# Kernel tuning notes

Hardware: AMD Instinct MI355X
Metric: run time of the kernel (lower is better)

Reference implementation:

```python
import jax, jax.numpy as jnp
import numpy as np
from jax import lax

T, B = 32, 32
GRID = (16, 16)
N_ACT = 5
CNN_DIM = 512
MAP_DIM = CNN_DIM + N_ACT  # 517
FLAT = MAP_DIM * GRID[0] * GRID[1]  # 132352


def _conv(x, w, b, stride):
    y = lax.conv_general_dilated(x, w, (stride, stride), 'VALID',
                                 dimension_numbers=('NCHW', 'OIHW', 'NCHW'))
    return jax.nn.relu(y + b[None, :, None, None])


def setup_inputs() -> dict:
    key = jax.random.key(0)
    ks = jax.random.split(key, 16)
    inp = {
        'image': jax.random.uniform(ks[0], (T * B, 3, 64, 64), jnp.float32),
        'last_action': jax.random.randint(ks[1], (T * B,), 0, N_ACT),
        'position': jax.random.randint(ks[2], (T * B, 2), 0, GRID[0]),
        'done': jnp.zeros((T, B), jnp.float32),
        'state0': jnp.zeros((B, MAP_DIM, GRID[0], GRID[1]), jnp.float32),
        'c1_w': jax.random.normal(ks[3], (32, 3, 8, 8), jnp.float32) * 0.05,
        'c1_b': jnp.zeros((32,), jnp.float32),
        'c2_w': jax.random.normal(ks[4], (64, 32, 4, 4), jnp.float32) * 0.05,
        'c2_b': jnp.zeros((64,), jnp.float32),
        'c3_w': jax.random.normal(ks[5], (64, 64, 3, 3), jnp.float32) * 0.05,
        'c3_b': jnp.zeros((64,), jnp.float32),
        'fc_w': jax.random.normal(ks[6], (CNN_DIM, 1024), jnp.float32) * 0.03,
        'fc_b': jnp.zeros((CNN_DIM,), jnp.float32),
        'pol_w1': jax.random.normal(ks[7], (64, FLAT), jnp.float32) * 0.005,
        'pol_b1': jnp.zeros((64,), jnp.float32),
        'pol_w2': jax.random.normal(ks[8], (N_ACT, 64), jnp.float32) * 0.01,
        'pol_b2': jnp.zeros((N_ACT,), jnp.float32),
        'val_w1': jax.random.normal(ks[9], (64, FLAT), jnp.float32) * 0.005,
        'val_b1': jnp.zeros((64,), jnp.float32),
        'val_w2': jax.random.normal(ks[10], (1, 64), jnp.float32) * 0.01,
        'val_b2': jnp.zeros((1,), jnp.float32),
    }
    return inp


def reference(image, last_action, position, done, state0,
              c1_w, c1_b, c2_w, c2_b, c3_w, c3_b, fc_w, fc_b,
              pol_w1, pol_b1, pol_w2, pol_b2, val_w1, val_b1, val_w2, val_b2):
    # NatureCNN feature extractor (image already normalized to [0,1])
    x = _conv(image, c1_w, c1_b, 4)   # (TB,32,15,15)
    x = _conv(x, c2_w, c2_b, 2)       # (TB,64,6,6)
    x = _conv(x, c3_w, c3_b, 1)       # (TB,64,4,4)
    feat = jax.nn.relu(x.reshape(x.shape[0], -1) @ fc_w.T + fc_b)  # (TB,512)
    onehot = jax.nn.one_hot(last_action, N_ACT, dtype=feat.dtype)
    h = jnp.concatenate([feat, onehot], axis=1)       # (TB,517)

    h_seq = h.reshape(T, B, MAP_DIM)
    idx_seq = position.reshape(T, B, 2)
    benv = jnp.arange(B)

    def step(state, inp):
        ht, dt, it = inp
        masked = (1.0 - dt)[:, None, None, None] * state      # reset done envs
        new_state = masked.at[benv, :, it[:, 0], it[:, 1]].set(ht)  # scatter write
        return new_state, new_state.reshape(B, -1)

    final_state, outs = lax.scan(step, state0, (h_seq, done, idx_seq))
    hidden = outs.reshape(T * B, FLAT)

    logits = jnp.tanh(hidden @ pol_w1.T + pol_b1) @ pol_w2.T + pol_b2  # (TB,5)
    v = jnp.tanh(hidden @ val_w1.T + val_b1) @ val_w2.T + val_b2       # (TB,1)
    return logits, v, final_state
```

## Files before the change

### kernel.cpp

```cpp
#include <hip/hip_runtime.h>

#define T_ 32
#define B_ 32
#define MAPD 517
#define P_ 256
#define FLATD (MAPD*P_)
#define TBN (T_*B_)

typedef unsigned short u16;
typedef unsigned int u32;
typedef __attribute__((ext_vector_type(4))) short short4v;
typedef __attribute__((ext_vector_type(8))) short short8v;
typedef __attribute__((ext_vector_type(4))) float f32x4;
typedef __attribute__((ext_vector_type(2))) float f32x2;
typedef __attribute__((ext_vector_type(4))) u32 u32x4;

__device__ __forceinline__ float bfv(u16 u){ u32 x = ((u32)u)<<16; return __uint_as_float(x); }
__device__ __forceinline__ u16 fbf(float f){
  u32 x = __float_as_uint(f);
  return (u16)((x + 0x7fffu + ((x>>16)&1u))>>16);
}
template<bool F32> __device__ __forceinline__ float ld(const void* p, size_t i){
  if constexpr (F32) return ((const float*)p)[i];
  else               return bfv(((const u16*)p)[i]);
}

__global__ void k_probe(const void* img, int* flag){
  if (threadIdx.x == 0 && blockIdx.x == 0){
    const u16* u = (const u16*)img;
    int cnt = 0;
    for (int i = 0; i < 256; ++i) if (u[i] <= 0x4380u) ++cnt;
    *flag = (cnt < 240) ? 1 : 0;
  }
}

__global__ __launch_bounds__(256) void k_prep(const void* c1w, const void* c2w, const void* c3w,
                                              const void* fcw, const void* st0,
                                              u16* W1F, u16* W2F, u16* W3F, u16* FWF, u16* ST0T,
                                              const int* flag){
  __shared__ __align__(16) char smem_[32768];
  bool f32 = (*flag != 0);
  int bid = blockIdx.x, tid = threadIdx.x;
  if (bid < 24){
    int idx = bid*256 + tid;
    int j = idx & 7, l = (idx>>3) & 63, t = idx>>9;
    int nt = t/6, s = t - nt*6;
    int oc = nt*16 + (l&15);
    int kk = 8*(4*s + (l>>4)) + j;
    float v = f32 ? ((const float*)c1w)[oc*192+kk] : bfv(((const u16*)c1w)[oc*192+kk]);
    W1F[idx] = fbf(v);
  } else if (bid < 152){
    int idx = (bid-24)*256 + tid;
    int j = idx & 7, l = (idx>>3) & 63, s = (idx>>9) & 15, nt = idx>>13;
    int oc = nt*16 + (l&15);
    int cin = (l>>4)*8 + j;
    int src = oc*512 + cin*16 + (s>>2)*4 + (s&3);
    float v = f32 ? ((const float*)c2w)[src] : bfv(((const u16*)c2w)[src]);
    W2F[idx] = fbf(v);
  } else if (bid < 296){
    int idx = (bid-152)*256 + tid;
    int j = idx & 7, l = (idx>>3) & 63, t = idx>>9;
    int nt = t/18, s = t - nt*18;
    int oc = nt*16 + (l&15);
    int c = (s&1)*32 + (l>>4)*8 + j;
    int src = oc*576 + c*9 + (s>>1);
    float v = f32 ? ((const float*)c3w)[src] : bfv(((const u16*)c3w)[src]);
    W3F[idx] = fbf(v);
  } else if (bid < 424){
    int b = bid - 296;
    for (int it = 0; it < 16; ++it){
      int idx = (b*16 + it)*256 + tid;
      int j = idx & 7, l = (idx>>3) & 63, frag = idx >> 9;
      int nt = frag >> 5, kt = frag & 31;
      int kc = kt*32 + ((l>>4)<<3) + j;
      int kr = (kc & 63)*16 + (kc >> 6);
      int o  = nt*16 + (l & 15);
      float v = f32 ? ((const float*)fcw)[(size_t)o*1024 + kr]
                    : bfv(((const u16*)fcw)[(size_t)o*1024 + kr]);
      FWF[idx] = fbf(v);
    }
  } else {
    u16* tile = (u16*)smem_;
    int b0 = bid - 424;
    int c0 = (b0 >> 2)*8, p0 = (b0 & 3)*64;
    for (int it = 0; it < 64; ++it){
      int idx = it*256 + tid;
      int pl = idx & 63, b = (idx>>6)&31, ci = idx>>11;
      int c = c0 + ci;
      float v = 0.f;
      if (c < MAPD)
        v = f32 ? ((const float*)st0)[((size_t)b*MAPD+c)*256 + p0+pl]
                : bfv(((const u16*)st0)[((size_t)b*MAPD+c)*256 + p0+pl]);
      tile[ci*2048 + pl*32 + b] = fbf(v);
    }
    __syncthreads();
    for (int it = 0; it < 64; ++it){
      int idx = it*256 + tid;
      int b = idx & 31, ci = (idx>>5)&7, pl = idx>>8;
      int c = c0 + ci;
      if (c < MAPD)
        ST0T[((size_t)(p0+pl)*MAPD + c)*32 + b] = tile[ci*2048 + pl*32 + b];
    }
  }
}

__global__ void k_meta(const int* pos, const void* done, const int* lact,
                       int* prev, float* coef, float* H, int* lastw, float* lastc, const int* flag){
  bool f32 = (*flag != 0);
  int bid = blockIdx.x;
  if (bid < 4){
    int i = bid*256 + threadIdx.x;
    int t = i >> 5, b = i & 31;
    int p = pos[i*2]*16 + pos[i*2+1];
    int pv = -1;
    for (int s = t-1; s >= 0; --s){
      int n = s*32 + b;
      if (pos[n*2]*16 + pos[n*2+1] == p){ pv = s; break; }
    }
    float cf = 1.f;
    for (int s = (pv<0?0:pv+1); s <= t-1; ++s)
      cf *= (1.f - (f32 ? ((const float*)done)[s*32+b] : bfv(((const u16*)done)[s*32+b])));
    prev[i] = pv; coef[i] = cf;
    int la = lact[i];
    #pragma unroll
    for (int a = 0; a < 5; ++a) H[(size_t)i*MAPD + 512 + a] = (la == a) ? 1.f : 0.f;
  } else {
    int i = (bid-4)*256 + threadIdx.x;
    int b = i >> 8, p = i & 255;
    int lw = -1;
    for (int s = T_-1; s >= 0; --s){
      int n = s*32 + b;
      if (pos[n*2]*16 + pos[n*2+1] == p){ lw = s; break; }
    }
    float cf = 1.f;
    for (int s = (lw<0?0:lw+1); s < T_; ++s)
      cf *= (1.f - (f32 ? ((const float*)done)[s*32+b] : bfv(((const u16*)done)[s*32+b])));
    lastw[i] = lw; lastc[i] = cf;
  }
}

__global__ __launch_bounds__(256) void k_conv123(const void* img,
                                                 const u16* __restrict__ W1F, const void* b1,
                                                 const u16* __restrict__ W2F, const void* b2,
                                                 const u16* __restrict__ W3F, const void* b3,
                                                 u16* __restrict__ out, const int* flag){
  __shared__ __align__(16) u16 smem[19488];
  u16* sImg = smem;
  u16* sA   = smem + 12288;
  u16* sBv  = smem;
  bool f32 = (*flag != 0);
  int n = blockIdx.x, tid = threadIdx.x;
  if (f32){
    const float4* ip = (const float4*)((const float*)img + (size_t)n*12288);
    for (int i = tid; i < 3072; i += 256){
      float4 v = ip[i];
      ushort4 u; u.x = fbf(v.x); u.y = fbf(v.y); u.z = fbf(v.z); u.w = fbf(v.w);
      int L = i*4;
      int addr = (L & ~63) | (((L & 63) + (((L >> 6) & 3) << 4)) & 63);
      *(ushort4*)(sImg + addr) = u;
    }
  } else {
    const ushort4* ip = (const ushort4*)((const u16*)img + (size_t)n*12288);
    for (int i = tid; i < 3072; i += 256){
      ushort4 u = ip[i];
      int L = i*4;
      int addr = (L & ~63) | (((L & 63) + (((L >> 6) & 3) << 4)) & 63);
      *(ushort4*)(sImg + addr) = u;
    }
  }
  int wv = tid >> 6, lane = tid & 63;
  int mi = lane & 15, q = lane >> 4;

  short8v bfr1[2][6];
  #pragma unroll
  for (int nt = 0; nt < 2; ++nt)
    #pragma unroll
    for (int s = 0; s < 6; ++s)
      bfr1[nt][s] = ((const short8v*)W1F)[(nt*6+s)*64 + lane];
  float b1v[2];
  #pragma unroll
  for (int nt = 0; nt < 2; ++nt)
    b1v[nt] = f32 ? ((const float*)b1)[nt*16+mi] : bfv(((const u16*)b1)[nt*16+mi]);
  __syncthreads();

  {
    f32x4 acc[4][2];
    #pragma unroll
    for (int mt = 0; mt < 4; ++mt)
      #pragma unroll
      for (int nt = 0; nt < 2; ++nt)
        acc[mt][nt] = (f32x4){0.f,0.f,0.f,0.f};
    int base[4];
    #pragma unroll
    for (int mt = 0; mt < 4; ++mt){
      int m = (wv*4+mt)*16 + mi;
      int mc = m < 225 ? m : 224;
      int oy = mc/15, ox = mc - oy*15;
      base[mt] = oy*256 + ox*4;
    }
    for (int s = 0; s < 6; ++s){
      int cky = 4*s + q;
      int off = (cky >> 3)*4096 + (cky & 7)*64;
      #pragma unroll
      for (int mt = 0; mt < 4; ++mt){
        int Lb = base[mt] + off;
        const u16* rp = sImg + (Lb & ~63);
        int x0 = Lb & 63;
        int rot = ((Lb >> 6) & 3) << 4;
        short4v lo = *(const short4v*)(rp + ((x0 + rot) & 63));
        short4v hi = *(const short4v*)(rp + ((x0 + 4 + rot) & 63));
        short8v a = __builtin_shufflevector(lo, hi, 0,1,2,3,4,5,6,7);
        acc[mt][0] = __builtin_amdgcn_mfma_f32_16x16x32_bf16(a, bfr1[0][s], acc[mt][0], 0,0,0);
        acc[mt][1] = __builtin_amdgcn_mfma_f32_16x16x32_bf16(a, bfr1[1][s], acc[mt][1], 0,0,0);
      }
    }
    __syncthreads();
    #pragma unroll
    for (int mt = 0; mt < 4; ++mt){
      int mrow0 = (wv*4+mt)*16 + q*4;
      #pragma unroll
      for (int nt = 0; nt < 2; ++nt){
        int oc = nt*16 + mi;
        #pragma unroll
        for (int r = 0; r < 4; ++r){
          int m = mrow0 + r;
          if (m < 225){
            int g = ((oc >> 3) ^ ((m >> 1) & 3)) << 3;
            sA[m*32 + g + (oc & 7)] = fbf(fmaxf(acc[mt][nt][r] + b1v[nt], 0.f));
          }
        }
      }
    }
  }
  __syncthreads();

  {
    short8v bfr2[16];
    #pragma unroll
    for (int s = 0; s < 16; ++s)
      bfr2[s] = ((const short8v*)W2F)[(wv*16+s)*64 + lane];
    int oc = wv*16 + mi;
    float bv = f32 ? ((const float*)b2)[oc] : bfv(((const u16*)b2)[oc]);
    f32x4 acc[3];
    #pragma unroll
    for (int mt = 0; mt < 3; ++mt) acc[mt] = (f32x4){0.f,0.f,0.f,0.f};
    int pixb[3];
    #pragma unroll
    for (int mt = 0; mt < 3; ++mt){
      int m = mt*16 + mi; if (m > 35) m = 35;
      int oy = m/6, ox = m - oy*6;
      pixb[mt] = oy*30 + ox*2;
    }
    #pragma unroll
    for (int s = 0; s < 16; ++s){
      int dp = (s>>2)*15 + (s&3);
      #pragma unroll
      for (int mt = 0; mt < 3; ++mt){
        int pix = pixb[mt] + dp;
        int g = (q ^ ((pix >> 1) & 3)) << 3;
        short8v a = *(const short8v*)(sA + pix*32 + g);
        acc[mt] = __builtin_amdgcn_mfma_f32_16x16x32_bf16(a, bfr2[s], acc[mt], 0,0,0);
      }
    }
    __syncthreads();
    #pragma unroll
    for (int mt = 0; mt < 3; ++mt)
      #pragma unroll
      for (int r = 0; r < 4; ++r){
        int m = mt*16 + q*4 + r;
        if (m < 36){
          int g = ((oc >> 3) ^ (m & 7)) << 3;
          sBv[m*64 + g + (oc & 7)] = fbf(fmaxf(acc[mt][r] + bv, 0.f));
        }
      }
  }
  __syncthreads();

  {
    int oy = mi >> 2, ox = mi & 3;
    int oc = wv*16 + mi;
    float bv = f32 ? ((const float*)b3)[oc] : bfv(((const u16*)b3)[oc]);
    short8v bfr3[18];
    #pragma unroll
    for (int s = 0; s < 18; ++s)
      bfr3[s] = ((const short8v*)W3F)[(wv*18+s)*64 + lane];
    f32x4 acc = (f32x4){0.f,0.f,0.f,0.f};
    #pragma unroll
    for (int s = 0; s < 18; ++s){
      int pair = s >> 1, ky = pair/3, kx = pair - ky*3;
      int pix = (oy+ky)*6 + ox+kx;
      int g = ((((s & 1) << 2) | q) ^ (pix & 7)) << 3;
      short8v a = *(const short8v*)(sBv + pix*64 + g);
      acc = __builtin_amdgcn_mfma_f32_16x16x32_bf16(a, bfr3[s], acc, 0,0,0);
    }
    u16* ob = out + (size_t)n*1024;
    #pragma unroll
    for (int r = 0; r < 4; ++r)
      ob[(q*4+r)*64 + oc] = fbf(fmaxf(acc[r] + bv, 0.f));
  }
}

__global__ __launch_bounds__(256) void k_fc(const u16* __restrict__ C, const u16* __restrict__ FWF,
                                            const void* fb, float* __restrict__ H, const int* flag){
  bool f32 = (*flag != 0);
  int wv = threadIdx.x >> 6, lane = threadIdx.x & 63;
  int mi = lane & 15, q = lane >> 4;
  int mt = blockIdx.x >> 3;
  int nt = (blockIdx.x & 7)*4 + wv;
  const u16* ap = C + (size_t)(mt*16 + mi)*1024 + q*8;
  const short8v* bp = (const short8v*)FWF + (size_t)nt*32*64 + lane;
  f32x4 acc0 = (f32x4){0.f,0.f,0.f,0.f};
  f32x4 acc1 = (f32x4){0.f,0.f,0.f,0.f};
  #pragma unroll
  for (int kt = 0; kt < 32; kt += 2){
    short8v a0 = *(const short8v*)(ap + kt*32);
    short8v b0 = bp[kt*64];
    short8v a1 = *(const short8v*)(ap + (kt+1)*32);
    short8v b1 = bp[(kt+1)*64];
    acc0 = __builtin_amdgcn_mfma_f32_16x16x32_bf16(a0, b0, acc0, 0,0,0);
    acc1 = __builtin_amdgcn_mfma_f32_16x16x32_bf16(a1, b1, acc1, 0,0,0);
  }
  int o = nt*16 + mi;
  float bv = f32 ? ((const float*)fb)[o] : bfv(((const u16*)fb)[o]);
  #pragma unroll
  for (int r = 0; r < 4; ++r){
    int m = mt*16 + q*4 + r;
    H[(size_t)m*MAPD + o] = fmaxf(acc0[r] + acc1[r] + bv, 0.f);
  }
}

template<bool F32> __device__ void wt_body(const void* pw1, const void* vw1, u16* wt, u32* tile){
  int c  = blockIdx.x >> 1;
  int ph = blockIdx.x & 1;
  for (int it = 0; it < 4; ++it){
    int idx = it*256 + threadIdx.x;
    int jp = idx >> 4, pg = idx & 15;
    int j0 = jp*2;
    const void* w = (j0 < 64) ? pw1 : vw1;
    int jj0 = (j0 < 64) ? j0 : j0-64;
    size_t base0 = (size_t)jj0*FLATD + c*P_ + ph*128 + pg*8;
    size_t base1 = base0 + FLATD;
    u16 a[8], b[8];
    if constexpr (F32){
      const float* f = (const float*)w;
      float4 a0 = *(const float4*)(f + base0), a1 = *(const float4*)(f + base0 + 4);
      float4 b0 = *(const float4*)(f + base1), b1 = *(const float4*)(f + base1 + 4);
      a[0]=fbf(a0.x); a[1]=fbf(a0.y); a[2]=fbf(a0.z); a[3]=fbf(a0.w);
      a[4]=fbf(a1.x); a[5]=fbf(a1.y); a[6]=fbf(a1.z); a[7]=fbf(a1.w);
      b[0]=fbf(b0.x); b[1]=fbf(b0.y); b[2]=fbf(b0.z); b[3]=fbf(b0.w);
      b[4]=fbf(b1.x); b[5]=fbf(b1.y); b[6]=fbf(b1.z); b[7]=fbf(b1.w);
    } else {
      short8v va = *(const short8v*)((const u16*)w + base0);
      short8v vb = *(const short8v*)((const u16*)w + base1);
      #pragma unroll
      for (int k = 0; k < 8; ++k){ a[k] = (u16)va[k]; b[k] = (u16)vb[k]; }
    }
    int slot = (jp >> 2) ^ pg;
    int sub  = jp & 3;
    #pragma unroll
    for (int k = 0; k < 8; ++k){
      int pp = pg*8 + k;
      tile[pp*64 + slot*4 + sub] = (u32)a[k] | ((u32)b[k] << 16);
    }
  }
  __syncthreads();
  for (int it = 0; it < 8; ++it){
    int idx = it*256 + threadIdx.x;
    int pp = idx >> 4, jb = idx & 15;
    int slot = jb ^ ((pp >> 3) & 15);
    u32x4 v = *(const u32x4*)(tile + pp*64 + slot*4);
    int p = ph*128 + pp;
    *(u32x4*)(wt + ((size_t)p*MAPD + c)*128 + jb*8) = v;
  }
}
__global__ __launch_bounds__(256) void k_wt(const void* pw1, const void* vw1, u16* wt, const int* flag){
  __shared__ u32 tile[128*64];
  if (*flag) wt_body<true>(pw1,vw1,wt,tile); else wt_body<false>(pw1,vw1,wt,tile);
}

template<int CLEN>
__device__ __forceinline__ void yloop(const u16* __restrict__ wp, const float* __restrict__ sSb,
                                      float (&acc)[8][2]){
  #pragma unroll 10
  for (int c = 0; c < CLEN; ++c){
    u32 w = *(const u32*)(wp + (size_t)c*128);
    float w0 = bfv((u16)(w & 0xffffu)), w1 = bfv((u16)(w >> 16));
    const float4* s4 = (const float4*)(sSb + c*32);
    float4 sa = s4[0], sb = s4[1];
    float sv[8] = {sa.x,sa.y,sa.z,sa.w,sb.x,sb.y,sb.z,sb.w};
    #pragma unroll
    for (int bb = 0; bb < 8; ++bb){
      acc[bb][0] += sv[bb]*w0;
      acc[bb][1] += sv[bb]*w1;
    }
  }
}
__global__ __launch_bounds__(256) void k_yinit(const u16* __restrict__ ST0T, const u16* __restrict__ wt,
                                               u16* __restrict__ PARTB){
  __shared__ float sS[130*32];
  int p = blockIdx.x >> 2, cq = blockIdx.x & 3;
  int c0 = cq*130;
  int clen = (cq == 3) ? 127 : 130;
  const ushort4* ssrc = (const ushort4*)(ST0T + ((size_t)p*MAPD + c0)*32);
  int n4 = clen*8;
  for (int i = threadIdx.x; i < n4; i += 256){
    ushort4 u = ssrc[i];
    float4 f; f.x = bfv(u.x); f.y = bfv(u.y); f.z = bfv(u.z); f.w = bfv(u.w);
    *(float4*)(sS + i*4) = f;
  }
  __syncthreads();
  int jg = threadIdx.x & 63, bg = threadIdx.x >> 6;
  int j0 = jg*2, b0 = bg*8;
  const u16* wp = wt + ((size_t)p*MAPD + c0)*128 + j0;
  float acc[8][2] = {};
  if (cq < 3) yloop<130>(wp, sS + b0, acc);
  else        yloop<127>(wp, sS + b0, acc);
  u32* op = (u32*)(PARTB + (size_t)blockIdx.x*4096);
  #pragma unroll
  for (int bb = 0; bb < 8; ++bb){
    u32 pk = (u32)fbf(acc[bb][0]) | ((u32)fbf(acc[bb][1]) << 16);
    op[((b0+bb)*128 + j0) >> 1] = pk;
  }
}

__global__ __launch_bounds__(256) void k_yred(const u16* __restrict__ PARTB, float* __restrict__ YI){
  int o = blockIdx.x*64 + (threadIdx.x & 63);
  int kq = threadIdx.x >> 6;
  float s = 0.f;
  const u16* pp = PARTB + (size_t)kq*256*4096 + o;
  #pragma unroll 8
  for (int k = 0; k < 256; ++k) s += bfv(pp[(size_t)k*4096]);
  __shared__ float red[256];
  red[threadIdx.x] = s;
  __syncthreads();
  if (threadIdx.x < 64)
    YI[o] = red[threadIdx.x] + red[threadIdx.x+64] + red[threadIdx.x+128] + red[threadIdx.x+192];
}

__global__ __launch_bounds__(128) void k_delta(const float* __restrict__ H, const u16* __restrict__ wt,
                                               const u16* __restrict__ st0t,
                                               const int* __restrict__ pos, const void* done,
                                               const int* __restrict__ prev, const float* __restrict__ coef,
                                               float* __restrict__ dlt8, const int* flag){
  __shared__ float diff[132];
  bool f32 = (*flag != 0);
  int n = blockIdx.x >> 2, cq = blockIdx.x & 3;
  int c0 = cq*130, clen = (cq == 3) ? 127 : 130;
  int b = n & 31;
  int p = pos[n*2]*16 + pos[n*2+1];
  float dn = f32 ? ((const float*)done)[n] : bfv(((const u16*)done)[n]);
  float m = 1.f - dn;
  int pv = prev[n];
  float cf = coef[n]*m;
  const float* hc = H + (size_t)n*MAPD + c0;
  for (int c = threadIdx.x; c < clen; c += 128){
    float old;
    if (pv >= 0) old = H[(size_t)(pv*32 + b)*MAPD + c0 + c];
    else         old = bfv(st0t[((size_t)p*MAPD + c0 + c)*32 + b]);
    diff[c] = hc[c] - cf*old;
  }
  __syncthreads();
  int half = threadIdx.x >> 6, jp = threadIdx.x & 63, j0 = jp*2;
  int hbase, hlen;
  if (cq == 3){ hbase = half*64; hlen = half ? 63 : 64; }
  else        { hbase = half*65; hlen = 65; }
  const u16* wp = wt + ((size_t)p*MAPD + c0 + hbase)*128 + j0;
  const float* dptr = diff + hbase;
  float a0 = 0.f, a1 = 0.f;
  int c = 0;
  for (; c + 4 <= hlen; c += 4){
    u32 w0 = *(const u32*)(wp + (size_t)(c+0)*128);
    u32 w1 = *(const u32*)(wp + (size_t)(c+1)*128);
    u32 w2 = *(const u32*)(wp + (size_t)(c+2)*128);
    u32 w3 = *(const u32*)(wp + (size_t)(c+3)*128);
    float d0 = dptr[c], d1 = dptr[c+1], d2 = dptr[c+2], d3 = dptr[c+3];
    a0 += d0*bfv((u16)(w0 & 0xffffu)) + d1*bfv((u16)(w1 & 0xffffu))
        + d2*bfv((u16)(w2 & 0xffffu)) + d3*bfv((u16)(w3 & 0xffffu));
    a1 += d0*bfv((u16)(w0 >> 16)) + d1*bfv((u16)(w1 >> 16))
        + d2*bfv((u16)(w2 >> 16)) + d3*bfv((u16)(w3 >> 16));
  }
  for (; c < hlen; ++c){
    u32 w = *(const u32*)(wp + (size_t)c*128);
    a0 += dptr[c]*bfv((u16)(w & 0xffffu));
    a1 += dptr[c]*bfv((u16)(w >> 16));
  }
  f32x2 st; st[0] = a0; st[1] = a1;
  *(f32x2*)(dlt8 + ((size_t)blockIdx.x*2 + half)*128 + j0) = st;
}

__global__ __launch_bounds__(128) void k_scan(const float* __restrict__ yi,
                                              const float* __restrict__ dlt8, const void* done,
                                              const void* pb1, const void* vb1,
                                              float* __restrict__ TH, const int* flag){
  bool f32 = (*flag != 0);
  int b = blockIdx.x, j = threadIdx.x;
  float y = yi[b*128 + j];
  float bias = (j < 64) ? (f32 ? ((const float*)pb1)[j]    : bfv(((const u16*)pb1)[j]))
                        : (f32 ? ((const float*)vb1)[j-64] : bfv(((const u16*)vb1)[j-64]));
  for (int t = 0; t < T_; ++t){
    int n = t*32 + b;
    float m = 1.f - (f32 ? ((const float*)done)[n] : bfv(((const u16*)done)[n]));
    const float* dp = dlt8 + (size_t)n*1024 + j;
    float d = dp[0] + dp[128] + dp[256] + dp[384]
            + dp[512] + dp[640] + dp[768] + dp[896];
    y = m*y + d;
    TH[(size_t)n*128 + j] = tanhf(y + bias);
  }
}

__global__ __launch_bounds__(256) void k_heads(const float* __restrict__ TH,
                                               const void* pw2, const void* pb2,
                                               const void* vw2, const void* vb2,
                                               void* out, const int* flag){
  bool f32 = (*flag != 0);
  int wv = threadIdx.x >> 6, lane = threadIdx.x & 63;
  int n = blockIdx.x*4 + wv;
  const float* th = TH + (size_t)n*128;
  float tq = th[lane];
  float tv = th[64 + lane];
  float acc[6];
  #pragma unroll
  for (int j = 0; j < 5; ++j)
    acc[j] = tq * (f32 ? ((const float*)pw2)[j*64 + lane] : bfv(((const u16*)pw2)[j*64 + lane]));
  acc[5] = tv * (f32 ? ((const float*)vw2)[lane] : bfv(((const u16*)vw2)[lane]));
  #pragma unroll
  for (int off = 32; off > 0; off >>= 1)
    #pragma unroll
    for (int j = 0; j < 6; ++j)
      acc[j] += __shfl_down(acc[j], off, 64);
  if (lane == 0){
    #pragma unroll
    for (int j = 0; j < 5; ++j){
      float s = acc[j] + (f32 ? ((const float*)pb2)[j] : bfv(((const u16*)pb2)[j]));
      if (f32) ((float*)out)[n*5 + j] = s; else ((u16*)out)[n*5 + j] = fbf(s);
    }
    float s = acc[5] + (f32 ? ((const float*)vb2)[0] : bfv(((const u16*)vb2)[0]));
    if (f32) ((float*)out)[5120 + n] = s; else ((u16*)out)[5120 + n] = fbf(s);
  }
}

template<bool F32> __device__ void final_body(const float* H, const void* st0,
                                              const int* lastw, const float* lastc, void* out){
  size_t i = (size_t)blockIdx.x*256 + threadIdx.x;
  if (i >= (size_t)B_*FLATD) return;
  int b = (int)(i / FLATD);
  int r = (int)(i - (size_t)b*FLATD);
  int c = r >> 8, p = r & 255;
  int lw = lastw[b*256 + p];
  float lc = lastc[b*256 + p];
  float v;
  if (lw >= 0) v = H[(size_t)(lw*32 + b)*MAPD + c]*lc;
  else         v = ld<F32>(st0, i)*lc;
  if constexpr (F32) ((float*)out)[6144 + i] = v; else ((u16*)out)[6144 + i] = fbf(v);
}
__global__ __launch_bounds__(256) void k_final(const float* H, const void* st0,
                                               const int* lastw, const float* lastc, void* out,
                                               const int* flag){
  if (*flag) final_body<true>(H,st0,lastw,lastc,out); else final_body<false>(H,st0,lastw,lastc,out);
}

extern "C" void kernel_launch(void* const* d_in, const int* in_sizes, int n_in,
                              void* d_out, int out_size, void* d_ws, size_t ws_size,
                              hipStream_t stream) {
  (void)in_sizes; (void)n_in; (void)out_size; (void)ws_size;
  const void* image = d_in[0];
  const int*  lact  = (const int*)d_in[1];
  const int*  pos   = (const int*)d_in[2];
  const void* done  = d_in[3];
  const void* st0   = d_in[4];
  const void* c1w = d_in[5];  const void* c1b = d_in[6];
  const void* c2w = d_in[7];  const void* c2b = d_in[8];
  const void* c3w = d_in[9];  const void* c3b = d_in[10];
  const void* fcw = d_in[11]; const void* fcb = d_in[12];
  const void* pw1 = d_in[13]; const void* pb1 = d_in[14];
  const void* pw2 = d_in[15]; const void* pb2 = d_in[16];
  const void* vw1 = d_in[17]; const void* vb1 = d_in[18];
  const void* vw2 = d_in[19]; const void* vb2 = d_in[20];
  char* ws = (char*)d_ws;

  u16*   WT    = (u16*)  (ws + 0);
  u16*   C     = (u16*)  (ws + 19464192);
  float* H     = (float*)(ws + 33882368);
  float* YI    = (float*)(ws + 36000256);
  u16*   PARTB = (u16*)  (ws + 36016640);
  float* DLT8  = (float*)(ws + 36016640);
  int*   PREV  = (int*)  (ws + 44405248);
  float* COEF  = (float*)(ws + 44409344);
  int*   LASTW = (int*)  (ws + 44413440);
  float* LASTC = (float*)(ws + 44446208);
  int*   FLAG  = (int*)  (ws + 44478976);
  u16*   W1F   = (u16*)  (ws + 44479232);
  u16*   W2F   = (u16*)  (ws + 44491520);
  u16*   W3F   = (u16*)  (ws + 44557056);
  u16*   FWF   = (u16*)  (ws + 44630784);
  u16*   ST0T  = (u16*)  (ws + 45679360);
  float* TH    = (float*)(ws + 54149888);

  k_probe<<<1, 64, 0, stream>>>(image, FLAG);
  k_prep <<<684, 256, 0, stream>>>(c1w, c2w, c3w, fcw, st0, W1F, W2F, W3F, FWF, ST0T, FLAG);
  k_meta <<<36, 256, 0, stream>>>(pos, done, lact, PREV, COEF, H, LASTW, LASTC, FLAG);
  k_conv123<<<1024, 256, 0, stream>>>(image, W1F, c1b, W2F, c2b, W3F, c3b, C, FLAG);
  k_fc   <<<512, 256, 0, stream>>>(C, FWF, fcb, H, FLAG);
  k_wt   <<<1034, 256, 0, stream>>>(pw1, vw1, WT, FLAG);
  k_yinit<<<1024, 256, 0, stream>>>(ST0T, WT, PARTB);
  k_yred <<<64, 256, 0, stream>>>(PARTB, YI);
  k_delta<<<4096, 128, 0, stream>>>(H, WT, ST0T, pos, done, PREV, COEF, DLT8, FLAG);
  k_scan <<<32, 128, 0, stream>>>(YI, DLT8, done, pb1, vb1, TH, FLAG);
  k_heads<<<256, 256, 0, stream>>>(TH, pw2, pb2, vw2, vb2, d_out, FLAG);
  k_final<<<16544, 256, 0, stream>>>(H, st0, LASTW, LASTC, d_out, FLAG);
}
```

Before: 368.0 us.

## Merge independent kernels into fewer launches and inline dtype probe per block

Merges twelve launches into five by grouping independent work into block-range partitions of combined kernels: weight transforms with prep and metadata, the y-init matmul with the fc layer, delta with y-reduction, and scan+heads with the final-state write. The dtype probe kernel is replaced by a per-wave ballot-style reduction inside each kernel, and head outputs are computed inside the scan via wave shuffles instead of a separate pass through a TH buffer. This removes launch gaps and serialization between independent stages and one intermediate buffer round trip. The cost is redundant probe loads in every block and possible load imbalance between heterogeneous block roles.

Measured after the change: 353.0 us. 4.1% less time.

```diff
diff --git a/kernel.cpp b/kernel.cpp
--- a/kernel.cpp
+++ b/kernel.cpp
@@ -24,314 +24,23 @@
   if constexpr (F32) return ((const float*)p)[i];
   else               return bfv(((const u16*)p)[i]);
 }
-
-__global__ void k_probe(const void* img, int* flag){
-  if (threadIdx.x == 0 && blockIdx.x == 0){
-    const u16* u = (const u16*)img;
-    int cnt = 0;
-    for (int i = 0; i < 256; ++i) if (u[i] <= 0x4380u) ++cnt;
-    *flag = (cnt < 240) ? 1 : 0;
-  }
-}
-
-__global__ __launch_bounds__(256) void k_prep(const void* c1w, const void* c2w, const void* c3w,
-                                              const void* fcw, const void* st0,
-                                              u16* W1F, u16* W2F, u16* W3F, u16* FWF, u16* ST0T,
-                                              const int* flag){
-  __shared__ __align__(16) char smem_[32768];
-  bool f32 = (*flag != 0);
-  int bid = blockIdx.x, tid = threadIdx.x;
-  if (bid < 24){
-    int idx = bid*256 + tid;
-    int j = idx & 7, l = (idx>>3) & 63, t = idx>>9;
-    int nt = t/6, s = t - nt*6;
-    int oc = nt*16 + (l&15);
-    int kk = 8*(4*s + (l>>4)) + j;
-    float v = f32 ? ((const float*)c1w)[oc*192+kk] : bfv(((const u16*)c1w)[oc*192+kk]);
-    W1F[idx] = fbf(v);
-  } else if (bid < 152){
-    int idx = (bid-24)*256 + tid;
-    int j = idx & 7, l = (idx>>3) & 63, s = (idx>>9) & 15, nt = idx>>13;
-    int oc = nt*16 + (l&15);
-    int cin = (l>>4)*8 + j;
-    int src = oc*512 + cin*16 + (s>>2)*4 + (s&3);
-    float v = f32 ? ((const float*)c2w)[src] : bfv(((const u16*)c2w)[src]);
-    W2F[idx] = fbf(v);
-  } else if (bid < 296){
-    int idx = (bid-152)*256 + tid;
-    int j = idx & 7, l = (idx>>3) & 63, t = idx>>9;
-    int nt = t/18, s = t - nt*18;
-    int oc = nt*16 + (l&15);
-    int c = (s&1)*32 + (l>>4)*8 + j;
-    int src = oc*576 + c*9 + (s>>1);
-    float v = f32 ? ((const float*)c3w)[src] : bfv(((const u16*)c3w)[src]);
-    W3F[idx] = fbf(v);
-  } else if (bid < 424){
-    int b = bid - 296;
-    for (int it = 0; it < 16; ++it){
-      int idx = (b*16 + it)*256 + tid;
-      int j = idx & 7, l = (idx>>3) & 63, frag = idx >> 9;
-      int nt = frag >> 5, kt = frag & 31;
-      int kc = kt*32 + ((l>>4)<<3) + j;
-      int kr = (kc & 63)*16 + (kc >> 6);
-      int o  = nt*16 + (l & 15);
-      float v = f32 ? ((const float*)fcw)[(size_t)o*1024 + kr]
-                    : bfv(((const u16*)fcw)[(size_t)o*1024 + kr]);
-      FWF[idx] = fbf(v);
-    }
-  } else {
-    u16* tile = (u16*)smem_;
-    int b0 = bid - 424;
-    int c0 = (b0 >> 2)*8, p0 = (b0 & 3)*64;
-    for (int it = 0; it < 64; ++it){
-      int idx = it*256 + tid;
-      int pl = idx & 63, b = (idx>>6)&31, ci = idx>>11;
-      int c = c0 + ci;
-      float v = 0.f;
-      if (c < MAPD)
-        v = f32 ? ((const float*)st0)[((size_t)b*MAPD+c)*256 + p0+pl]
-                : bfv(((const u16*)st0)[((size_t)b*MAPD+c)*256 + p0+pl]);
-      tile[ci*2048 + pl*32 + b] = fbf(v);
-    }
-    __syncthreads();
-    for (int it = 0; it < 64; ++it){
-      int idx = it*256 + tid;
-      int b = idx & 31, ci = (idx>>5)&7, pl = idx>>8;
-      int c = c0 + ci;
-      if (c < MAPD)
-        ST0T[((size_t)(p0+pl)*MAPD + c)*32 + b] = tile[ci*2048 + pl*32 + b];
-    }
-  }
-}
-
-__global__ void k_meta(const int* pos, const void* done, const int* lact,
-                       int* prev, float* coef, float* H, int* lastw, float* lastc, const int* flag){
-  bool f32 = (*flag != 0);
-  int bid = blockIdx.x;
-  if (bid < 4){
-    int i = bid*256 + threadIdx.x;
-    int t = i >> 5, b = i & 31;
-    int p = pos[i*2]*16 + pos[i*2+1];
-    int pv = -1;
-    for (int s = t-1; s >= 0; --s){
-      int n = s*32 + b;
-      if (pos[n*2]*16 + pos[n*2+1] == p){ pv = s; break; }
-    }
-    float cf = 1.f;
-    for (int s = (pv<0?0:pv+1); s <= t-1; ++s)
-      cf *= (1.f - (f32 ? ((const float*)done)[s*32+b] : bfv(((const u16*)done)[s*32+b])));
-    prev[i] = pv; coef[i] = cf;
-    int la = lact[i];
-    #pragma unroll
-    for (int a = 0; a < 5; ++a) H[(size_t)i*MAPD + 512 + a] = (la == a) ? 1.f : 0.f;
-  } else {
-    int i = (bid-4)*256 + threadIdx.x;
-    int b = i >> 8, p = i & 255;
-    int lw = -1;
-    for (int s = T_-1; s >= 0; --s){
-      int n = s*32 + b;
-      if (pos[n*2]*16 + pos[n*2+1] == p){ lw = s; break; }
-    }
-    float cf = 1.f;
-    for (int s = (lw<0?0:lw+1); s < T_; ++s)
-      cf *= (1.f - (f32 ? ((const float*)done)[s*32+b] : bfv(((const u16*)done)[s*32+b])));
-    lastw[i] = lw; lastc[i] = cf;
-  }
-}
-
-__global__ __launch_bounds__(256) void k_conv123(const void* img,
-                                                 const u16* __restrict__ W1F, const void* b1,
-                                                 const u16* __restrict__ W2F, const void* b2,
-                                                 const u16* __restrict__ W3F, const void* b3,
-                                                 u16* __restrict__ out, const int* flag){
-  __shared__ __align__(16) u16 smem[19488];
-  u16* sImg = smem;
-  u16* sA   = smem + 12288;
-  u16* sBv  = smem;
-  bool f32 = (*flag != 0);
-  int n = blockIdx.x, tid = threadIdx.x;
-  if (f32){
-    const float4* ip = (const float4*)((const float*)img + (size_t)n*12288);
-    for (int i = tid; i < 3072; i += 256){
-      float4 v = ip[i];
-      ushort4 u; u.x = fbf(v.x); u.y = fbf(v.y); u.z = fbf(v.z); u.w = fbf(v.w);
-      int L = i*4;
-      int addr = (L & ~63) | (((L & 63) + (((L >> 6) & 3) << 4)) & 63);
-      *(ushort4*)(sImg + addr) = u;
-    }
-  } else {
-    const ushort4* ip = (const ushort4*)((const u16*)img + (size_t)n*12288);
-    for (int i = tid; i < 3072; i += 256){
-      ushort4 u = ip[i];
-      int L = i*4;
-      int addr = (L & ~63) | (((L & 63) + (((L >> 6) & 3) << 4)) & 63);
-      *(ushort4*)(sImg + addr) = u;
-    }
-  }
-  int wv = tid >> 6, lane = tid & 63;
-  int mi = lane & 15, q = lane >> 4;
-
-  short8v bfr1[2][6];
+__device__ __forceinline__ float ldf(bool f32, const void* p, size_t i){
+  return f32 ? ((const float*)p)[i] : bfv(((const u16*)p)[i]);
+}
+
+__device__ __forceinline__ bool probe_f32(const void* img){
+  int lane = threadIdx.x & 63;
+  ushort4 v = ((const ushort4*)img)[lane];
+  int c = (v.x <= 0x4380u) + (v.y <= 0x4380u) + (v.z <= 0x4380u) + (v.w <= 0x4380u);
   #pragma unroll
-  for (int nt = 0; nt < 2; ++nt)
-    #pragma unroll
-    for (int s = 0; s < 6; ++s)
-      bfr1[nt][s] = ((const short8v*)W1F)[(nt*6+s)*64 + lane];
-  float b1v[2];
-  #pragma unroll
-  for (int nt = 0; nt < 2; ++nt)
-    b1v[nt] = f32 ? ((const float*)b1)[nt*16+mi] : bfv(((const u16*)b1)[nt*16+mi]);
-  __syncthreads();
-
-  {
-    f32x4 acc[4][2];
-    #pragma unroll
-    for (int mt = 0; mt < 4; ++mt)
-      #pragma unroll
-      for (int nt = 0; nt < 2; ++nt)
-        acc[mt][nt] = (f32x4){0.f,0.f,0.f,0.f};
-    int base[4];
-    #pragma unroll
-    for (int mt = 0; mt < 4; ++mt){
-      int m = (wv*4+mt)*16 + mi;
-      int mc = m < 225 ? m : 224;
-      int oy = mc/15, ox = mc - oy*15;
-      base[mt] = oy*256 + ox*4;
-    }
-    for (int s = 0; s < 6; ++s){
-      int cky = 4*s + q;
-      int off = (cky >> 3)*4096 + (cky & 7)*64;
-      #pragma unroll
-      for (int mt = 0; mt < 4; ++mt){
-        int Lb = base[mt] + off;
-        const u16* rp = sImg + (Lb & ~63);
-        int x0 = Lb & 63;
-        int rot = ((Lb >> 6) & 3) << 4;
-        short4v lo = *(const short4v*)(rp + ((x0 + rot) & 63));
-        short4v hi = *(const short4v*)(rp + ((x0 + 4 + rot) & 63));
-        short8v a = __builtin_shufflevector(lo, hi, 0,1,2,3,4,5,6,7);
-        acc[mt][0] = __builtin_amdgcn_mfma_f32_16x16x32_bf16(a, bfr1[0][s], acc[mt][0], 0,0,0);
-        acc[mt][1] = __builtin_amdgcn_mfma_f32_16x16x32_bf16(a, bfr1[1][s], acc[mt][1], 0,0,0);
-      }
-    }
-    __syncthreads();
-    #pragma unroll
-    for (int mt = 0; mt < 4; ++mt){
-      int mrow0 = (wv*4+mt)*16 + q*4;
-      #pragma unroll
-      for (int nt = 0; nt < 2; ++nt){
-        int oc = nt*16 + mi;
-        #pragma unroll
-        for (int r = 0; r < 4; ++r){
-          int m = mrow0 + r;
-          if (m < 225){
-            int g = ((oc >> 3) ^ ((m >> 1) & 3)) << 3;
-            sA[m*32 + g + (oc & 7)] = fbf(fmaxf(acc[mt][nt][r] + b1v[nt], 0.f));
-          }
-        }
-      }
-    }
-  }
-  __syncthreads();
-
-  {
-    short8v bfr2[16];
-    #pragma unroll
-    for (int s = 0; s < 16; ++s)
-      bfr2[s] = ((const short8v*)W2F)[(wv*16+s)*64 + lane];
-    int oc = wv*16 + mi;
-    float bv = f32 ? ((const float*)b2)[oc] : bfv(((const u16*)b2)[oc]);
-    f32x4 acc[3];
-    #pragma unroll
-    for (int mt = 0; mt < 3; ++mt) acc[mt] = (f32x4){0.f,0.f,0.f,0.f};
-    int pixb[3];
-    #pragma unroll
-    for (int mt = 0; mt < 3; ++mt){
-      int m = mt*16 + mi; if (m > 35) m = 35;
-      int oy = m/6, ox = m - oy*6;
-      pixb[mt] = oy*30 + ox*2;
-    }
-    #pragma unroll
-    for (int s = 0; s < 16; ++s){
-      int dp = (s>>2)*15 + (s&3);
-      #pragma unroll
-      for (int mt = 0; mt < 3; ++mt){
-        int pix = pixb[mt] + dp;
-        int g = (q ^ ((pix >> 1) & 3)) << 3;
-        short8v a = *(const short8v*)(sA + pix*32 + g);
-        acc[mt] = __builtin_amdgcn_mfma_f32_16x16x32_bf16(a, bfr2[s], acc[mt], 0,0,0);
-      }
-    }
-    __syncthreads();
-    #pragma unroll
-    for (int mt = 0; mt < 3; ++mt)
-      #pragma unroll
-      for (int r = 0; r < 4; ++r){
-        int m = mt*16 + q*4 + r;
-        if (m < 36){
-          int g = ((oc >> 3) ^ (m & 7)) << 3;
-          sBv[m*64 + g + (oc & 7)] = fbf(fmaxf(acc[mt][r] + bv, 0.f));
-        }
-      }
-  }
-  __syncthreads();
-
-  {
-    int oy = mi >> 2, ox = mi & 3;
-    int oc = wv*16 + mi;
-    float bv = f32 ? ((const float*)b3)[oc] : bfv(((const u16*)b3)[oc]);
-    short8v bfr3[18];
-    #pragma unroll
-    for (int s = 0; s < 18; ++s)
-      bfr3[s] = ((const short8v*)W3F)[(wv*18+s)*64 + lane];
-    f32x4 acc = (f32x4){0.f,0.f,0.f,0.f};
-    #pragma unroll
-    for (int s = 0; s < 18; ++s){
-      int pair = s >> 1, ky = pair/3, kx = pair - ky*3;
-      int pix = (oy+ky)*6 + ox+kx;
-      int g = ((((s & 1) << 2) | q) ^ (pix & 7)) << 3;
-      short8v a = *(const short8v*)(sBv + pix*64 + g);
-      acc = __builtin_amdgcn_mfma_f32_16x16x32_bf16(a, bfr3[s], acc, 0,0,0);
-    }
-    u16* ob = out + (size_t)n*1024;
-    #pragma unroll
-    for (int r = 0; r < 4; ++r)
-      ob[(q*4+r)*64 + oc] = fbf(fmaxf(acc[r] + bv, 0.f));
-  }
-}
-
-__global__ __launch_bounds__(256) void k_fc(const u16* __restrict__ C, const u16* __restrict__ FWF,
-                                            const void* fb, float* __restrict__ H, const int* flag){
-  bool f32 = (*flag != 0);
-  int wv = threadIdx.x >> 6, lane = threadIdx.x & 63;
-  int mi = lane & 15, q = lane >> 4;
-  int mt = blockIdx.x >> 3;
-  int nt = (blockIdx.x & 7)*4 + wv;
-  const u16* ap = C + (size_t)(mt*16 + mi)*1024 + q*8;
-  const short8v* bp = (const short8v*)FWF + (size_t)nt*32*64 + lane;
-  f32x4 acc0 = (f32x4){0.f,0.f,0.f,0.f};
-  f32x4 acc1 = (f32x4){0.f,0.f,0.f,0.f};
-  #pragma unroll
-  for (int kt = 0; kt < 32; kt += 2){
-    short8v a0 = *(const short8v*)(ap + kt*32);
-    short8v b0 = bp[kt*64];
-    short8v a1 = *(const short8v*)(ap + (kt+1)*32);
-    short8v b1 = bp[(kt+1)*64];
-    acc0 = __builtin_amdgcn_mfma_f32_16x16x32_bf16(a0, b0, acc0, 0,0,0);
-    acc1 = __builtin_amdgcn_mfma_f32_16x16x32_bf16(a1, b1, acc1, 0,0,0);
-  }
-  int o = nt*16 + mi;
-  float bv = f32 ? ((const float*)fb)[o] : bfv(((const u16*)fb)[o]);
-  #pragma unroll
-  for (int r = 0; r < 4; ++r){
-    int m = mt*16 + q*4 + r;
-    H[(size_t)m*MAPD + o] = fmaxf(acc0[r] + acc1[r] + bv, 0.f);
-  }
-}
-
-template<bool F32> __device__ void wt_body(const void* pw1, const void* vw1, u16* wt, u32* tile){
-  int c  = blockIdx.x >> 1;
-  int ph = blockIdx.x & 1;
+  for (int off = 32; off > 0; off >>= 1) c += __shfl_xor(c, off, 64);
+  return c < 240;
+}
+
+template<bool F32> __device__ void wt_body(int lbid, const void* pw1, const void* vw1,
+                                           u16* wt, u32* tile){
+  int c  = lbid >> 1;
+  int ph = lbid & 1;
   for (int it = 0; it < 4; ++it){
     int idx = it*256 + threadIdx.x;
     int jp = idx >> 4, pg = idx & 15;
@@ -373,9 +82,280 @@
     *(u32x4*)(wt + ((size_t)p*MAPD + c)*128 + jb*8) = v;
   }
 }
-__global__ __launch_bounds__(256) void k_wt(const void* pw1, const void* vw1, u16* wt, const int* flag){
-  __shared__ u32 tile[128*64];
-  if (*flag) wt_body<true>(pw1,vw1,wt,tile); else wt_body<false>(pw1,vw1,wt,tile);
+
+__device__ void prep_body(bool f32, int bid, const void* c1w, const void* c2w, const void* c3w,
+                          const void* fcw, const void* st0,
+                          u16* W1F, u16* W2F, u16* W3F, u16* FWF, u16* ST0T, char* smem_){
+  int tid = threadIdx.x;
+  if (bid < 24){
+    int idx = bid*256 + tid;
+    int j = idx & 7, l = (idx>>3) & 63, t = idx>>9;
+    int nt = t/6, s = t - nt*6;
+    int oc = nt*16 + (l&15);
+    int kk = 8*(4*s + (l>>4)) + j;
+    float v = ldf(f32, c1w, oc*192+kk);
+    W1F[idx] = fbf(v);
+  } else if (bid < 152){
+    int idx = (bid-24)*256 + tid;
+    int j = idx & 7, l = (idx>>3) & 63, s = (idx>>9) & 15, nt = idx>>13;
+    int oc = nt*16 + (l&15);
+    int cin = (l>>4)*8 + j;
+    int src = oc*512 + cin*16 + (s>>2)*4 + (s&3);
+    W2F[idx] = fbf(ldf(f32, c2w, src));
+  } else if (bid < 296){
+    int idx = (bid-152)*256 + tid;
+    int j = idx & 7, l = (idx>>3) & 63, t = idx>>9;
+    int nt = t/18, s = t - nt*18;
+    int oc = nt*16 + (l&15);
+    int c = (s&1)*32 + (l>>4)*8 + j;
+    int src = oc*576 + c*9 + (s>>1);
+    W3F[idx] = fbf(ldf(f32, c3w, src));
+  } else if (bid < 424){
+    int b = bid - 296;
+    for (int it = 0; it < 16; ++it){
+      int idx = (b*16 + it)*256 + tid;
+      int j = idx & 7, l = (idx>>3) & 63, frag = idx >> 9;
+      int nt = frag >> 5, kt = frag & 31;
+      int kc = kt*32 + ((l>>4)<<3) + j;
+      int kr = (kc & 63)*16 + (kc >> 6);
+      int o  = nt*16 + (l & 15);
+      FWF[idx] = fbf(ldf(f32, fcw, (size_t)o*1024 + kr));
+    }
+  } else {
+    u16* tile = (u16*)smem_;
+    int b0 = bid - 424;
+    int c0 = (b0 >> 2)*8, p0 = (b0 & 3)*64;
+    for (int it = 0; it < 64; ++it){
+      int idx = it*256 + tid;
+      int pl = idx & 63, b = (idx>>6)&31, ci = idx>>11;
+      int c = c0 + ci;
+      float v = 0.f;
+      if (c < MAPD) v = ldf(f32, st0, ((size_t)b*MAPD+c)*256 + p0+pl);
+      tile[ci*2048 + pl*32 + b] = fbf(v);
+    }
+    __syncthreads();
+    for (int it = 0; it < 64; ++it){
+      int idx = it*256 + tid;
+      int b = idx & 31, ci = (idx>>5)&7, pl = idx>>8;
+      int c = c0 + ci;
+      if (c < MAPD)
+        ST0T[((size_t)(p0+pl)*MAPD + c)*32 + b] = tile[ci*2048 + pl*32 + b];
+    }
+  }
+}
+
+__device__ void meta_body(bool f32, int bid, const int* pos, const void* done, const int* lact,
+                          int* prev, float* coef, float* H, int* lastw, float* lastc){
+  if (bid < 4){
+    int i = bid*256 + threadIdx.x;
+    int t = i >> 5, b = i & 31;
+    int p = pos[i*2]*16 + pos[i*2+1];
+    int pv = -1;
+    for (int s = t-1; s >= 0; --s){
+      int n = s*32 + b;
+      if (pos[n*2]*16 + pos[n*2+1] == p){ pv = s; break; }
+    }
+    float cf = 1.f;
+    for (int s = (pv<0?0:pv+1); s <= t-1; ++s)
+      cf *= (1.f - ldf(f32, done, s*32+b));
+    prev[i] = pv; coef[i] = cf;
+    int la = lact[i];
+    #pragma unroll
+    for (int a = 0; a < 5; ++a) H[(size_t)i*MAPD + 512 + a] = (la == a) ? 1.f : 0.f;
+  } else {
+    int i = (bid-4)*256 + threadIdx.x;
+    int b = i >> 8, p = i & 255;
+    int lw = -1;
+    for (int s = T_-1; s >= 0; --s){
+      int n = s*32 + b;
+      if (pos[n*2]*16 + pos[n*2+1] == p){ lw = s; break; }
+    }
+    float cf = 1.f;
+    for (int s = (lw<0?0:lw+1); s < T_; ++s)
+      cf *= (1.f - ldf(f32, done, s*32+b));
+    lastw[i] = lw; lastc[i] = cf;
+  }
+}
+
+__global__ __launch_bounds__(256) void k_A(const void* image,
+                                           const void* pw1, const void* vw1, u16* wt,
+                                           const void* c1w, const void* c2w, const void* c3w,
+                                           const void* fcw, const void* st0,
+                                           u16* W1F, u16* W2F, u16* W3F, u16* FWF, u16* ST0T,
+                                           const int* pos, const void* done, const int* lact,
+                                           int* prev, float* coef, float* H, int* lastw, float* lastc){
+  __shared__ __align__(16) char smem_[32768];
+  bool f32 = probe_f32(image);
+  int bid = blockIdx.x;
+  if (bid < 1034){
+    if (f32) wt_body<true>(bid, pw1, vw1, wt, (u32*)smem_);
+    else     wt_body<false>(bid, pw1, vw1, wt, (u32*)smem_);
+  } else if (bid < 1718){
+    prep_body(f32, bid-1034, c1w, c2w, c3w, fcw, st0, W1F, W2F, W3F, FWF, ST0T, smem_);
+  } else {
+    meta_body(f32, bid-1718, pos, done, lact, prev, coef, H, lastw, lastc);
+  }
+}
+
+__global__ __launch_bounds__(256) void k_conv123(const void* img,
+                                                 const u16* __restrict__ W1F, const void* b1,
+                                                 const u16* __restrict__ W2F, const void* b2,
+                                                 const u16* __restrict__ W3F, const void* b3,
+                                                 u16* __restrict__ out){
+  __shared__ __align__(16) u16 smem[19488];
+  u16* sImg = smem;
+  u16* sA   = smem + 12288;
+  u16* sBv  = smem;
+  bool f32 = probe_f32(img);
+  int n = blockIdx.x, tid = threadIdx.x;
+  if (f32){
+    const float4* ip = (const float4*)((const float*)img + (size_t)n*12288);
+    for (int i = tid; i < 3072; i += 256){
+      float4 v = ip[i];
+      ushort4 u; u.x = fbf(v.x); u.y = fbf(v.y); u.z = fbf(v.z); u.w = fbf(v.w);
+      int L = i*4;
+      int addr = (L & ~63) | (((L & 63) + (((L >> 6) & 3) << 4)) & 63);
+      *(ushort4*)(sImg + addr) = u;
+    }
+  } else {
+    const ushort4* ip = (const ushort4*)((const u16*)img + (size_t)n*12288);
+    for (int i = tid; i < 3072; i += 256){
+      ushort4 u = ip[i];
+      int L = i*4;
+      int addr = (L & ~63) | (((L & 63) + (((L >> 6) & 3) << 4)) & 63);
+      *(ushort4*)(sImg + addr) = u;
+    }
+  }
+  int wv = tid >> 6, lane = tid & 63;
+  int mi = lane & 15, q = lane >> 4;
+
+  short8v bfr1[2][6];
+  #pragma unroll
+  for (int nt = 0; nt < 2; ++nt)
+    #pragma unroll
+    for (int s = 0; s < 6; ++s)
+      bfr1[nt][s] = ((const short8v*)W1F)[(nt*6+s)*64 + lane];
+  float b1v[2];
+  #pragma unroll
+  for (int nt = 0; nt < 2; ++nt)
+    b1v[nt] = ldf(f32, b1, nt*16+mi);
+  __syncthreads();
+
+  {
+    f32x4 acc[4][2];
+    #pragma unroll
+    for (int mt = 0; mt < 4; ++mt)
+      #pragma unroll
+      for (int nt = 0; nt < 2; ++nt)
+        acc[mt][nt] = (f32x4){0.f,0.f,0.f,0.f};
+    int base[4];
+    #pragma unroll
+    for (int mt = 0; mt < 4; ++mt){
+      int m = (wv*4+mt)*16 + mi;
+      int mc = m < 225 ? m : 224;
+      int oy = mc/15, ox = mc - oy*15;
+      base[mt] = oy*256 + ox*4;
+    }
+    for (int s = 0; s < 6; ++s){
+      int cky = 4*s + q;
+      int off = (cky >> 3)*4096 + (cky & 7)*64;
+      #pragma unroll
+      for (int mt = 0; mt < 4; ++mt){
+        int Lb = base[mt] + off;
+        const u16* rp = sImg + (Lb & ~63);
+        int x0 = Lb & 63;
+        int rot = ((Lb >> 6) & 3) << 4;
+        short4v lo = *(const short4v*)(rp + ((x0 + rot) & 63));
+        short4v hi = *(const short4v*)(rp + ((x0 + 4 + rot) & 63));
+        short8v a = __builtin_shufflevector(lo, hi, 0,1,2,3,4,5,6,7);
+        acc[mt][0] = __builtin_amdgcn_mfma_f32_16x16x32_bf16(a, bfr1[0][s], acc[mt][0], 0,0,0);
+        acc[mt][1] = __builtin_amdgcn_mfma_f32_16x16x32_bf16(a, bfr1[1][s], acc[mt][1], 0,0,0);
+      }
+    }
+    __syncthreads();
+    #pragma unroll
+    for (int mt = 0; mt < 4; ++mt){
+      int mrow0 = (wv*4+mt)*16 + q*4;
+      #pragma unroll
+      for (int nt = 0; nt < 2; ++nt){
+        int oc = nt*16 + mi;
+        #pragma unroll
+        for (int r = 0; r < 4; ++r){
+          int m = mrow0 + r;
+          if (m < 225){
+            int g = ((oc >> 3) ^ ((m >> 1) & 3)) << 3;
+            sA[m*32 + g + (oc & 7)] = fbf(fmaxf(acc[mt][nt][r] + b1v[nt], 0.f));
+          }
+        }
+      }
+    }
+  }
+  __syncthreads();
+
+  {
+    short8v bfr2[16];
+    #pragma unroll
+    for (int s = 0; s < 16; ++s)
+      bfr2[s] = ((const short8v*)W2F)[(wv*16+s)*64 + lane];
+    int oc = wv*16 + mi;
+    float bv = ldf(f32, b2, oc);
+    f32x4 acc[3];
+    #pragma unroll
+    for (int mt = 0; mt < 3; ++mt) acc[mt] = (f32x4){0.f,0.f,0.f,0.f};
+    int pixb[3];
+    #pragma unroll
+    for (int mt = 0; mt < 3; ++mt){
+      int m = mt*16 + mi; if (m > 35) m = 35;
+      int oy = m/6, ox = m - oy*6;
+      pixb[mt] = oy*30 + ox*2;
+    }
+    #pragma unroll
+    for (int s = 0; s < 16; ++s){
+      int dp = (s>>2)*15 + (s&3);
+      #pragma unroll
+      for (int mt = 0; mt < 3; ++mt){
+        int pix = pixb[mt] + dp;
+        int g = (q ^ ((pix >> 1) & 3)) << 3;
+        short8v a = *(const short8v*)(sA + pix*32 + g);
+        acc[mt] = __builtin_amdgcn_mfma_f32_16x16x32_bf16(a, bfr2[s], acc[mt], 0,0,0);
+      }
+    }
+    __syncthreads();
+    #pragma unroll
+    for (int mt = 0; mt < 3; ++mt)
+      #pragma unroll
+      for (int r = 0; r < 4; ++r){
+        int m = mt*16 + q*4 + r;
+        if (m < 36){
+          int g = ((oc >> 3) ^ (m & 7)) << 3;
+          sBv[m*64 + g + (oc & 7)] = fbf(fmaxf(acc[mt][r] + bv, 0.f));
+        }
+      }
+  }
+  __syncthreads();
+
+  {
+    int oy = mi >> 2, ox = mi & 3;
+    int oc = wv*16 + mi;
+    float bv = ldf(f32, b3, oc);
+    short8v bfr3[18];
+    #pragma unroll
+    for (int s = 0; s < 18; ++s)
+      bfr3[s] = ((const short8v*)W3F)[(wv*18+s)*64 + lane];
+    f32x4 acc = (f32x4){0.f,0.f,0.f,0.f};
+    #pragma unroll
+    for (int s = 0; s < 18; ++s){
+      int pair = s >> 1, ky = pair/3, kx = pair - ky*3;
+      int pix = (oy+ky)*6 + ox+kx;
+      int g = ((((s & 1) << 2) | q) ^ (pix & 7)) << 3;
+      short8v a = *(const short8v*)(sBv + pix*64 + g);
+      acc = __builtin_amdgcn_mfma_f32_16x16x32_bf16(a, bfr3[s], acc, 0,0,0);
+    }
+    u16* ob = out + (size_t)n*1024;
+    #pragma unroll
+    for (int r = 0; r < 4; ++r)
+      ob[(q*4+r)*64 + oc] = fbf(fmaxf(acc[r] + bv, 0.f));
+  }
 }
 
 template<int CLEN>
@@ -395,10 +375,9 @@
     }
   }
 }
-__global__ __launch_bounds__(256) void k_yinit(const u16* __restrict__ ST0T, const u16* __restrict__ wt,
-                                               u16* __restrict__ PARTB){
-  __shared__ float sS[130*32];
-  int p = blockIdx.x >> 2, cq = blockIdx.x & 3;
+__device__ void yinit_body(int lbid, const u16* __restrict__ ST0T, const u16* __restrict__ wt,
+                           u16* __restrict__ PARTB, float* sS){
+  int p = lbid >> 2, cq = lbid & 3;
   int c0 = cq*130;
   int clen = (cq == 3) ? 127 : 130;
   const ushort4* ssrc = (const ushort4*)(ST0T + ((size_t)p*MAPD + c0)*32);
@@ -415,52 +394,77 @@
   float acc[8][2] = {};
   if (cq < 3) yloop<130>(wp, sS + b0, acc);
   else        yloop<127>(wp, sS + b0, acc);
-  u32* op = (u32*)(PARTB + (size_t)blockIdx.x*4096);
+  u32* op = (u32*)(PARTB + (size_t)lbid*4096);
   #pragma unroll
   for (int bb = 0; bb < 8; ++bb){
     u32 pk = (u32)fbf(acc[bb][0]) | ((u32)fbf(acc[bb][1]) << 16);
     op[((b0+bb)*128 + j0) >> 1] = pk;
   }
 }
-
-__global__ __launch_bounds__(256) void k_yred(const u16* __restrict__ PARTB, float* __restrict__ YI){
-  int o = blockIdx.x*64 + (threadIdx.x & 63);
-  int kq = threadIdx.x >> 6;
-  float s = 0.f;
-  const u16* pp = PARTB + (size_t)kq*256*4096 + o;
-  #pragma unroll 8
-  for (int k = 0; k < 256; ++k) s += bfv(pp[(size_t)k*4096]);
-  __shared__ float red[256];
-  red[threadIdx.x] = s;
-  __syncthreads();
-  if (threadIdx.x < 64)
-    YI[o] = red[threadIdx.x] + red[threadIdx.x+64] + red[threadIdx.x+128] + red[threadIdx.x+192];
-}
-
-__global__ __launch_bounds__(128) void k_delta(const float* __restrict__ H, const u16* __restrict__ wt,
-                                               const u16* __restrict__ st0t,
-                                               const int* __restrict__ pos, const void* done,
-                                               const int* __restrict__ prev, const float* __restrict__ coef,
-                                               float* __restrict__ dlt8, const int* flag){
-  __shared__ float diff[132];
-  bool f32 = (*flag != 0);
-  int n = blockIdx.x >> 2, cq = blockIdx.x & 3;
+__device__ void fc_body(int lbid, bool f32, const u16* __restrict__ C, const u16* __restrict__ FWF,
+                        const void* fb, float* __restrict__ H){
+  int wv = threadIdx.x >> 6, lane = threadIdx.x & 63;
+  int mi = lane & 15, q = lane >> 4;
+  int mt = lbid >> 3;
+  int nt = (lbid & 7)*4 + wv;
+  const u16* ap = C + (size_t)(mt*16 + mi)*1024 + q*8;
+  const short8v* bp = (const short8v*)FWF + (size_t)nt*32*64 + lane;
+  f32x4 acc0 = (f32x4){0.f,0.f,0.f,0.f};
+  f32x4 acc1 = (f32x4){0.f,0.f,0.f,0.f};
+  #pragma unroll
+  for (int kt = 0; kt < 32; kt += 2){
+    short8v a0 = *(const short8v*)(ap + kt*32);
+    short8v b0 = bp[kt*64];
+    short8v a1 = *(const short8v*)(ap + (kt+1)*32);
+    short8v b1 = bp[(kt+1)*64];
+    acc0 = __builtin_amdgcn_mfma_f32_16x16x32_bf16(a0, b0, acc0, 0,0,0);
+    acc1 = __builtin_amdgcn_mfma_f32_16x16x32_bf16(a1, b1, acc1, 0,0,0);
+  }
+  int o = nt*16 + mi;
+  float bv = ldf(f32, fb, o);
+  #pragma unroll
+  for (int r = 0; r < 4; ++r){
+    int m = mt*16 + q*4 + r;
+    H[(size_t)m*MAPD + o] = fmaxf(acc0[r] + acc1[r] + bv, 0.f);
+  }
+}
+__global__ __launch_bounds__(256) void k_C(const void* image,
+                                           const u16* __restrict__ ST0T, const u16* __restrict__ wt,
+                                           u16* __restrict__ PARTB,
+                                           const u16* __restrict__ C, const u16* __restrict__ FWF,
+                                           const void* fb, float* __restrict__ H){
+  __shared__ float sS[130*32];
+  if (blockIdx.x < 1024){
+    yinit_body(blockIdx.x, ST0T, wt, PARTB, sS);
+  } else {
+    bool f32 = probe_f32(image);
+    fc_body(blockIdx.x - 1024, f32, C, FWF, fb, H);
+  }
+}
+
+__device__ void delta_body(int obid, int ltid, float* diff, bool f32,
+                           const float* __restrict__ H, const u16* __restrict__ wt,
+                           const u16* __restrict__ st0t,
+                           const int* __restrict__ pos, const void* done,
+                           const int* __restrict__ prev, const float* __restrict__ coef,
+                           float* __restrict__ dlt8){
+  int n = obid >> 2, cq = obid & 3;
   int c0 = cq*130, clen = (cq == 3) ? 127 : 130;
   int b = n & 31;
   int p = pos[n*2]*16 + pos[n*2+1];
-  float dn = f32 ? ((const float*)done)[n] : bfv(((const u16*)done)[n]);
+  float dn = ldf(f32, done, n);
   float m = 1.f - dn;
   int pv = prev[n];
   float cf = coef[n]*m;
   const float* hc = H + (size_t)n*MAPD + c0;
-  for (int c = threadIdx.x; c < clen; c += 128){
+  for (int c = ltid; c < clen; c += 128){
     float old;
     if (pv >= 0) old = H[(size_t)(pv*32 + b)*MAPD + c0 + c];
     else         old = bfv(st0t[((size_t)p*MAPD + c0 + c)*32 + b]);
     diff[c] = hc[c] - cf*old;
   }
   __syncthreads();
-  int half = threadIdx.x >> 6, jp = threadIdx.x & 63, j0 = jp*2;
+  int half = ltid >> 6, jp = ltid & 63, j0 = jp*2;
   int hbase, hlen;
   if (cq == 3){ hbase = half*64; hlen = half ? 63 : 64; }
   else        { hbase = half*65; hlen = 65; }
@@ -485,78 +489,116 @@
     a1 += dptr[c]*bfv((u16)(w >> 16));
   }
   f32x2 st; st[0] = a0; st[1] = a1;
-  *(f32x2*)(dlt8 + ((size_t)blockIdx.x*2 + half)*128 + j0) = st;
-}
-
-__global__ __launch_bounds__(128) void k_scan(const float* __restrict__ yi,
-                                              const float* __restrict__ dlt8, const void* done,
-                                              const void* pb1, const void* vb1,
-                                              float* __restrict__ TH, const int* flag){
-  bool f32 = (*flag != 0);
+  *(f32x2*)(dlt8 + ((size_t)obid*2 + half)*128 + j0) = st;
+}
+__global__ __launch_bounds__(256) void k_D(const void* image,
+                                           const float* __restrict__ H, const u16* __restrict__ wt,
+                                           const u16* __restrict__ st0t,
+                                           const int* __restrict__ pos, const void* done,
+                                           const int* __restrict__ prev, const float* __restrict__ coef,
+                                           float* __restrict__ dlt8,
+                                           const u16* __restrict__ PARTB, float* __restrict__ YI){
+  __shared__ float diff2[2][132];
+  __shared__ float red[256];
+  if (blockIdx.x < 2048){
+    bool f32 = probe_f32(image);
+    int sub = threadIdx.x >> 7;
+    int obid = blockIdx.x*2 + sub;
+    delta_body(obid, threadIdx.x & 127, diff2[sub], f32, H, wt, st0t, pos, done, prev, coef, dlt8);
+  } else {
+    int lbid = blockIdx.x - 2048;
+    int o = lbid*64 + (threadIdx.x & 63);
+    int kq = threadIdx.x >> 6;
+    float s = 0.f;
+    const u16* pp = PARTB + (size_t)kq*256*4096 + o;
+    #pragma unroll 8
+    for (int k = 0; k < 256; ++k) s += bfv(pp[(size_t)k*4096]);
+    red[threadIdx.x] = s;
+    __syncthreads();
+    if (threadIdx.x < 64)
+      YI[o] = red[threadIdx.x] + red[threadIdx.x+64] + red[threadIdx.x+128] + red[threadIdx.x+192];
+  }
+}
+
+__device__ void scan_heads_body(bool f32, const float* __restrict__ yi,
+                                const float* __restrict__ dlt8, const void* done,
+                                const void* pb1, const void* vb1,
+                                const void* pw2, const void* pb2,
+                                const void* vw2, const void* vb2, void* out){
   int b = blockIdx.x, j = threadIdx.x;
+  int lane = j & 63;
+  bool pol = j < 64;
   float y = yi[b*128 + j];
-  float bias = (j < 64) ? (f32 ? ((const float*)pb1)[j]    : bfv(((const u16*)pb1)[j]))
-                        : (f32 ? ((const float*)vb1)[j-64] : bfv(((const u16*)vb1)[j-64]));
+  float bias = pol ? ldf(f32, pb1, j) : ldf(f32, vb1, j-64);
+  float w2[5];
+  if (pol){
+    #pragma unroll
+    for (int jj = 0; jj < 5; ++jj) w2[jj] = ldf(f32, pw2, jj*64 + lane);
+  } else {
+    w2[0] = ldf(f32, vw2, lane);
+  }
   for (int t = 0; t < T_; ++t){
     int n = t*32 + b;
-    float m = 1.f - (f32 ? ((const float*)done)[n] : bfv(((const u16*)done)[n]));
+    float m = 1.f - ldf(f32, done, n);
     const float* dp = dlt8 + (size_t)n*1024 + j;
     float d = dp[0] + dp[128] + dp[256] + dp[384]
             + dp[512] + dp[640] + dp[768] + dp[896];
     y = m*y + d;
-    TH[(size_t)n*128 + j] = tanhf(y + bias);
-  }
-}
-
-__global__ __launch_bounds__(256) void k_heads(const float* __restrict__ TH,
-                                               const void* pw2, const void* pb2,
-                                               const void* vw2, const void* vb2,
-                                               void* out, const int* flag){
-  bool f32 = (*flag != 0);
-  int wv = threadIdx.x >> 6, lane = threadIdx.x & 63;
-  int n = blockIdx.x*4 + wv;
-  const float* th = TH + (size_t)n*128;
-  float tq = th[lane];
-  float tv = th[64 + lane];
-  float acc[6];
-  #pragma unroll
-  for (int j = 0; j < 5; ++j)
-    acc[j] = tq * (f32 ? ((const float*)pw2)[j*64 + lane] : bfv(((const u16*)pw2)[j*64 + lane]));
-  acc[5] = tv * (f32 ? ((const float*)vw2)[lane] : bfv(((const u16*)vw2)[lane]));
-  #pragma unroll
-  for (int off = 32; off > 0; off >>= 1)
-    #pragma unroll
-    for (int j = 0; j < 6; ++j)
-      acc[j] += __shfl_down(acc[j], off, 64);
-  if (lane == 0){
-    #pragma unroll
-    for (int j = 0; j < 5; ++j){
-      float s = acc[j] + (f32 ? ((const float*)pb2)[j] : bfv(((const u16*)pb2)[j]));
-      if (f32) ((float*)out)[n*5 + j] = s; else ((u16*)out)[n*5 + j] = fbf(s);
-    }
-    float s = acc[5] + (f32 ? ((const float*)vb2)[0] : bfv(((const u16*)vb2)[0]));
-    if (f32) ((float*)out)[5120 + n] = s; else ((u16*)out)[5120 + n] = fbf(s);
-  }
-}
-
-template<bool F32> __device__ void final_body(const float* H, const void* st0,
-                                              const int* lastw, const float* lastc, void* out){
-  size_t i = (size_t)blockIdx.x*256 + threadIdx.x;
-  if (i >= (size_t)B_*FLATD) return;
-  int b = (int)(i / FLATD);
-  int r = (int)(i - (size_t)b*FLATD);
-  int c = r >> 8, p = r & 255;
-  int lw = lastw[b*256 + p];
-  float lc = lastc[b*256 + p];
-  float v;
-  if (lw >= 0) v = H[(size_t)(lw*32 + b)*MAPD + c]*lc;
-  else         v = ld<F32>(st0, i)*lc;
-  if constexpr (F32) ((float*)out)[6144 + i] = v; else ((u16*)out)[6144 + i] = fbf(v);
-}
-__global__ __launch_bounds__(256) void k_final(const float* H, const void* st0,
-                                               const int* lastw, const float* lastc, void* out,
-                                               const int* flag){
-  if (*flag) final_body<true>(H,st0,lastw,lastc,out); else final_body<false>(H,st0,lastw,lastc,out);
+    float th = tanhf(y + bias);
+    if (pol){
+      float s0 = th*w2[0], s1 = th*w2[1], s2 = th*w2[2], s3 = th*w2[3], s4 = th*w2[4];
+      #pragma unroll
+      for (int off = 32; off > 0; off >>= 1){
+        s0 += __shfl_xor(s0, off, 64);
+        s1 += __shfl_xor(s1, off, 64);
+        s2 += __shfl_xor(s2, off, 64);
+        s3 += __shfl_xor(s3, off, 64);
+        s4 += __shfl_xor(s4, off, 64);
+      }
+      if (lane == 0){
+        float sv[5] = {s0,s1,s2,s3,s4};
+        #pragma unroll
+        for (int jj = 0; jj < 5; ++jj){
+          float s = sv[jj] + ldf(f32, pb2, jj);
+          if (f32) ((float*)out)[n*5 + jj] = s; else ((u16*)out)[n*5 + jj] = fbf(s);
+        }
+      }
+    } else {
+      float s = th*w2[0];
+      #pragma unroll
+      for (int off = 32; off > 0; off >>= 1) s += __shfl_xor(s, off, 64);
+      if (lane == 0){
+        s += ldf(f32, vb2, 0);
+        if (f32) ((float*)out)[5120 + n] = s; else ((u16*)out)[5120 + n] = fbf(s);
+      }
+    }
+  }
+}
+__global__ __launch_bounds__(256) void k_E(const void* image,
+                                           const float* __restrict__ yi, const float* __restrict__ dlt8,
+                                           const void* done, const void* pb1, const void* vb1,
+                                           const void* pw2, const void* pb2,
+                                           const void* vw2, const void* vb2,
+                                           const float* __restrict__ H, const void* st0,
+                                           const int* __restrict__ lastw, const float* __restrict__ lastc,
+                                           void* out){
+  bool f32 = probe_f32(image);
+  if (blockIdx.x < 32){
+    if (threadIdx.x >= 128) return;
+    scan_heads_body(f32, yi, dlt8, done, pb1, vb1, pw2, pb2, vw2, vb2, out);
+  } else {
+    size_t i = (size_t)(blockIdx.x - 32)*256 + threadIdx.x;
+    if (i >= (size_t)B_*FLATD) return;
+    int b = (int)(i / FLATD);
+    int r = (int)(i - (size_t)b*FLATD);
+    int c = r >> 8, p = r & 255;
+    int lw = lastw[b*256 + p];
+    float lc = lastc[b*256 + p];
+    float v;
+    if (lw >= 0) v = H[(size_t)(lw*32 + b)*MAPD + c]*lc;
+    else         v = ldf(f32, st0, i)*lc;
+    if (f32) ((float*)out)[6144 + i] = v; else ((u16*)out)[6144 + i] = fbf(v);
+  }
 }
 
 extern "C" void kernel_launch(void* const* d_in, const int* in_sizes, int n_in,
@@ -579,33 +621,27 @@
   char* ws = (char*)d_ws;
 
   u16*   WT    = (u16*)  (ws + 0);
-  u16*   C     = (u16*)  (ws + 19464192);
   float* H     = (float*)(ws + 33882368);
   float* YI    = (float*)(ws + 36000256);
   u16*   PARTB = (u16*)  (ws + 36016640);
-  float* DLT8  = (float*)(ws + 36016640);
   int*   PREV  = (int*)  (ws + 44405248);
   float* COEF  = (float*)(ws + 44409344);
   int*   LASTW = (int*)  (ws + 44413440);
   float* LASTC = (float*)(ws + 44446208);
-  int*   FLAG  = (int*)  (ws + 44478976);
   u16*   W1F   = (u16*)  (ws + 44479232);
   u16*   W2F   = (u16*)  (ws + 44491520);
   u16*   W3F   = (u16*)  (ws + 44557056);
   u16*   FWF   = (u16*)  (ws + 44630784);
   u16*   ST0T  = (u16*)  (ws + 45679360);
-  float* TH    = (float*)(ws + 54149888);
-
-  k_probe<<<1, 64, 0, stream>>>(image, FLAG);
-  k_prep <<<684, 256, 0, stream>>>(c1w, c2w, c3w, fcw, st0, W1F, W2F, W3F, FWF, ST0T, FLAG);
-  k_meta <<<36, 256, 0, stream>>>(pos, done, lact, PREV, COEF, H, LASTW, LASTC, FLAG);
-  k_conv123<<<1024, 256, 0, stream>>>(image, W1F, c1b, W2F, c2b, W3F, c3b, C, FLAG);
-  k_fc   <<<512, 256, 0, stream>>>(C, FWF, fcb, H, FLAG);
-  k_wt   <<<1034, 256, 0, stream>>>(pw1, vw1, WT, FLAG);
-  k_yinit<<<1024, 256, 0, stream>>>(ST0T, WT, PARTB);
-  k_yred <<<64, 256, 0, stream>>>(PARTB, YI);
-  k_delta<<<4096, 128, 0, stream>>>(H, WT, ST0T, pos, done, PREV, COEF, DLT8, FLAG);
-  k_scan <<<32, 128, 0, stream>>>(YI, DLT8, done, pb1, vb1, TH, FLAG);
-  k_heads<<<256, 256, 0, stream>>>(TH, pw2, pb2, vw2, vb2, d_out, FLAG);
-  k_final<<<16544, 256, 0, stream>>>(H, st0, LASTW, LASTC, d_out, FLAG);
-}
+  u16*   C     = (u16*)  (ws + 54149888);
+  float* DLT8  = (float*)(ws + 56247040);
+
+  k_A      <<<1754, 256, 0, stream>>>(image, pw1, vw1, WT, c1w, c2w, c3w, fcw, st0,
+                                      W1F, W2F, W3F, FWF, ST0T,
+                                      pos, done, lact, PREV, COEF, H, LASTW, LASTC);
+  k_conv123<<<1024, 256, 0, stream>>>(image, W1F, c1b, W2F, c2b, W3F, c3b, C);
+  k_C      <<<1536, 256, 0, stream>>>(image, ST0T, WT, PARTB, C, FWF, fcb, H);
+  k_D      <<<2112, 256, 0, stream>>>(image, H, WT, ST0T, pos, done, PREV, COEF, DLT8, PARTB, YI);
+  k_E      <<<16576, 256, 0, stream>>>(image, YI, DLT8, done, pb1, vb1, pw2, pb2, vw2, vb2,
+                                       H, st0, LASTW, LASTC, d_out);
+}
```
